# Optimization experiments

Hardware: AMD Instinct MI355X
Metric: run time of the kernel (lower is better)

The kernel has to match this reference:

```python
import jax, jax.numpy as jnp
import numpy as np

B, T, D_MODEL, HEAD_DIM = 16, 4096, 512, 64


def setup_inputs() -> dict:
    key = jax.random.key(0)
    kx, kq, kk, kv = jax.random.split(key, 4)
    x = jax.random.normal(kx, (B, T, D_MODEL), dtype=jnp.float32)
    # torch nn.Linear weights, stored pre-transposed as [in, out] for x @ W
    s = 1.0 / np.sqrt(D_MODEL)
    Wq = jax.random.uniform(kq, (D_MODEL, HEAD_DIM), jnp.float32, -s, s)
    Wk = jax.random.uniform(kk, (D_MODEL, HEAD_DIM), jnp.float32, -s, s)
    Wv = jax.random.uniform(kv, (D_MODEL, HEAD_DIM), jnp.float32, -s, s)
    return {"x": x, "Wq": Wq, "Wk": Wk, "Wv": Wv}


def reference(x, Wq, Wk, Wv):
    # Single-head causal self-attention (dropout in eval mode = identity)
    q = x @ Wq  # [B, T, h]
    k = x @ Wk
    v = x @ Wv
    scale = 1.0 / np.sqrt(HEAD_DIM).astype(np.float32)
    scores = jnp.einsum("bth,bsh->bts", q, k) * scale  # [B, T, T]
    t = scores.shape[1]
    causal = jnp.tril(jnp.ones((t, t), dtype=bool))
    scores = jnp.where(causal, scores, -jnp.inf)
    weights = jax.nn.softmax(scores, axis=-1)
    return jnp.einsum("bts,bsh->bth", weights, v)  # [B, T, h]
```

## Files before the change

### kernel.cpp

```cpp
#include <hip/hip_runtime.h>
#include <hip/hip_bf16.h>
#include <math.h>


#define NB 16
#define NT 4096
#define DMODEL 512
#define HD 64
#define CEXP 0.18033688011112042f

typedef unsigned short u16;
typedef unsigned int u32;
typedef __attribute__((ext_vector_type(2))) unsigned int u32x2;
typedef __attribute__((ext_vector_type(8))) short bf16x8;
typedef __attribute__((ext_vector_type(4))) float f32x4;
typedef __attribute__((ext_vector_type(16))) float f32x16;

__device__ __forceinline__ u16 f2bf(float x) {
  union { float f; unsigned u; } v; v.f = x;
  unsigned r = v.u + 0x7fffu + ((v.u >> 16) & 1u);
  return (u16)(r >> 16);
}

__device__ __forceinline__ u32 cvtpk(float lo, float hi) {
  u32 r;
  asm("v_cvt_pk_bf16_f32 %0, %1, %2" : "=v"(r) : "v"(lo), "v"(hi));
  return r;
}

__device__ __forceinline__ u32x2 lane_swap(u32 a, u32 b) {
  asm("v_permlane32_swap_b32 %0, %1" : "+v"(a), "+v"(b));
  u32x2 r; r[0] = a; r[1] = b; return r;
}

__device__ __forceinline__ void gload16(const void* g, void* l) {
  __builtin_amdgcn_global_load_lds(
      (const __attribute__((address_space(1))) void*)g,
      (__attribute__((address_space(3))) void*)l, 16, 0, 0);
}

#define MFMA32(a, b, c) __builtin_amdgcn_mfma_f32_16x16x32_bf16(a, b, c, 0, 0, 0)
#define WMFMA(a, b, c)  __builtin_amdgcn_mfma_f32_32x32x16_bf16(a, b, c, 0, 0, 0)
#define LD8(p) (*(const bf16x8*)(p))

__global__ void prep_wt(const float* __restrict__ Wq, const float* __restrict__ Wk,
                        const float* __restrict__ Wv, u16* __restrict__ Wt) {
  int k0 = blockIdx.x * 16;
  int t = threadIdx.x;
#pragma unroll
  for (int i = 0; i < 12; ++i) {
    int idx = t + i * 256;
    int n = idx % 192;
    int kk = idx / 192;
    const float* W = (n < 64) ? Wq : (n < 128) ? Wk : Wv;
    float w = W[(size_t)(k0 + kk) * 64 + (n & 63)];
    Wt[(size_t)n * 512 + k0 + kk] = f2bf(w);
  }
}

__global__ __launch_bounds__(512) void proj_qkv(const float* __restrict__ x,
                                                const u16* __restrict__ Wt,
                                                u16* __restrict__ qo,
                                                u16* __restrict__ ko,
                                                u16* __restrict__ vo) {
  __shared__ u16 As[128][48];
  int t = threadIdx.x;
  int m0 = blockIdx.x * 128;
  int lane = t & 63, wid = t >> 6;
  int wr = wid >> 2, wc = wid & 3;
  int g = lane >> 4, li = lane & 15;
  f32x4 acc[4][3];
#pragma unroll
  for (int i = 0; i < 4; ++i)
#pragma unroll
    for (int j = 0; j < 3; ++j) acc[i][j] = (f32x4){0.f, 0.f, 0.f, 0.f};

  int row = t >> 2, quad = t & 3;
  for (int k0 = 0; k0 < 512; k0 += 32) {
    __syncthreads();
    const float* src = x + (size_t)(m0 + row) * DMODEL + k0 + quad * 8;
    float4 f0 = *(const float4*)src;
    float4 f1 = *(const float4*)(src + 4);
    union { u16 s[8]; bf16x8 v; } tmp;
    tmp.s[0] = f2bf(f0.x); tmp.s[1] = f2bf(f0.y);
    tmp.s[2] = f2bf(f0.z); tmp.s[3] = f2bf(f0.w);
    tmp.s[4] = f2bf(f1.x); tmp.s[5] = f2bf(f1.y);
    tmp.s[6] = f2bf(f1.z); tmp.s[7] = f2bf(f1.w);
    *(bf16x8*)&As[row][quad * 8] = tmp.v;
    __syncthreads();

    bf16x8 a[4], bb[3];
#pragma unroll
    for (int mf = 0; mf < 4; ++mf)
      a[mf] = *(const bf16x8*)&As[wr * 64 + mf * 16 + li][g * 8];
#pragma unroll
    for (int nf = 0; nf < 3; ++nf)
      bb[nf] = *(const bf16x8*)(Wt + (size_t)(wc * 48 + nf * 16 + li) * 512 + k0 + g * 8);
#pragma unroll
    for (int mf = 0; mf < 4; ++mf)
#pragma unroll
      for (int nf = 0; nf < 3; ++nf)
        acc[mf][nf] = MFMA32(a[mf], bb[nf], acc[mf][nf]);
  }

#pragma unroll
  for (int nf = 0; nf < 3; ++nf) {
    int n = wc * 48 + nf * 16 + li;
    if (n < 64) {
      int col = n;
#pragma unroll
      for (int mf = 0; mf < 4; ++mf)
#pragma unroll
        for (int r = 0; r < 4; ++r) {
          int m = m0 + wr * 64 + mf * 16 + 4 * g + r;
          qo[(size_t)m * HD + col] = f2bf(acc[mf][nf][r] * CEXP);
        }
    } else if (n < 128) {
      int col = n & 63;
      int dt = col >> 4, hh = (col >> 3) & 1, jj = col & 7;
      size_t fo = (size_t)(dt * 2 + hh) * 256 + jj;
#pragma unroll
      for (int mf = 0; mf < 4; ++mf)
#pragma unroll
        for (int r = 0; r < 4; ++r) {
          int m = m0 + wr * 64 + mf * 16 + 4 * g + r;
          ko[(size_t)(m >> 5) * 2048 + fo + (m & 31) * 8] = f2bf(acc[mf][nf][r]);
        }
    } else {
      int d = n - 128;
      int dh = d >> 5, l31d = d & 31;
#pragma unroll
      for (int mf = 0; mf < 4; ++mf) {
        int mbase = m0 + wr * 64 + mf * 16 + 4 * g;
        int kk2 = mbase & 31;
        int kt2 = kk2 >> 4, hh = (kk2 >> 3) & 1;
        size_t off = (size_t)(mbase >> 5) * 2048 +
                     (size_t)((dh * 2 + kt2) * 2 + hh) * 256 + l31d * 8 + (mbase & 7);
        ushort4 pk;
        pk.x = f2bf(acc[mf][nf][0]);
        pk.y = f2bf(acc[mf][nf][1]);
        pk.z = f2bf(acc[mf][nf][2]);
        pk.w = f2bf(acc[mf][nf][3]);
        *(ushort4*)(vo + off) = pk;
      }
    }
  }
}

__global__ __launch_bounds__(256, 4) void attn_fwd10(const u16* __restrict__ qg,
                                                     const u16* __restrict__ kg,
                                                     const u16* __restrict__ vg,
                                                     float* __restrict__ out) {
  __shared__ __align__(16) char smem[33792];
  u16* KV = (u16*)smem;
  float* MrgF = (float*)smem;

  int tid = threadIdx.x;
  int lane = tid & 63, w = tid >> 6;
  int l31 = lane & 31, h = lane >> 5;
  int qi = w >> 1, ki = w & 1;

  int f = blockIdx.x;
  int xcd = f & 7, i = f >> 3;
  int m = i >> 5, cu = i & 31;
  int b, bp;
  if (m == 0)      { b = 2 * xcd;     bp = 63 - cu; }
  else if (m == 1) { b = 2 * xcd;     bp = 31 - cu; }
  else if (m == 2) { b = 2 * xcd + 1; bp = cu;      }
  else             { b = 2 * xcd + 1; bp = 32 + cu; }

  const int diag = 2 * bp + qi;
  const int nr = bp + 1;
  const int q0w = bp * 64 + qi * 32;

  const u16* qb = qg + (size_t)b * NT * HD;
  const u16* kbs = kg + (size_t)b * NT * HD;
  const u16* vbs = vg + (size_t)b * NT * HD;
  float* ob = out + (size_t)b * NT * HD;

  bf16x8 qf[4];
#pragma unroll
  for (int dt = 0; dt < 4; ++dt)
    qf[dt] = LD8(qb + (size_t)(q0w + l31) * HD + dt * 16 + 8 * h);

  f32x16 oacc0, oacc1;
#pragma unroll
  for (int r = 0; r < 16; ++r) { oacc0[r] = 0.f; oacc1[r] = 0.f; }
  float lsum = 0.f;

  auto COMPUTE = [&](const u16* kp0, const u16* vp0, bool maskdiag) {
    bf16x8 kf[4], vf[4];
#pragma unroll
    for (int dt = 0; dt < 4; ++dt)
      kf[dt] = LD8(kp0 + dt * 512 + h * 256 + l31 * 8);
#pragma unroll
    for (int dv = 0; dv < 4; ++dv)
      vf[dv] = LD8(vp0 + dv * 512 + h * 256 + l31 * 8);

    f32x16 sv;
#pragma unroll
    for (int r = 0; r < 16; ++r) sv[r] = 0.f;
    sv = WMFMA(kf[0], qf[0], sv);
    sv = WMFMA(kf[1], qf[1], sv);
    sv = WMFMA(kf[2], qf[2], sv);
    sv = WMFMA(kf[3], qf[3], sv);

    if (maskdiag) {
#pragma unroll
      for (int r = 0; r < 16; ++r) {
        int key = (r & 3) + 8 * (r >> 2) + 4 * h;
        if (key > l31) sv[r] = -1e30f;
      }
    }

    float p[16];
#pragma unroll
    for (int r = 0; r < 16; ++r) p[r] = __builtin_amdgcn_exp2f(sv[r]);
    lsum += (((p[0] + p[1]) + (p[2] + p[3])) + ((p[4] + p[5]) + (p[6] + p[7]))) +
            (((p[8] + p[9]) + (p[10] + p[11])) + ((p[12] + p[13]) + (p[14] + p[15])));
    u32 A0 = cvtpk(p[0], p[1]),   A1 = cvtpk(p[2], p[3]);
    u32 B0 = cvtpk(p[4], p[5]),   B1 = cvtpk(p[6], p[7]);
    u32 C0 = cvtpk(p[8], p[9]),   C1 = cvtpk(p[10], p[11]);
    u32 E0 = cvtpk(p[12], p[13]), E1 = cvtpk(p[14], p[15]);
    u32x2 s0 = lane_swap(A0, B0), s1 = lane_swap(A1, B1);
    u32x2 s2 = lane_swap(C0, E0), s3 = lane_swap(C1, E1);
    union { u32 d[4]; bf16x8 v; } f0u, f1u;
    f0u.d[0] = s0[0]; f0u.d[1] = s1[0]; f0u.d[2] = s0[1]; f0u.d[3] = s1[1];
    f1u.d[0] = s2[0]; f1u.d[1] = s3[0]; f1u.d[2] = s2[1]; f1u.d[3] = s3[1];

    oacc0 = WMFMA(vf[0], f0u.v, oacc0);
    oacc1 = WMFMA(vf[2], f0u.v, oacc1);
    oacc0 = WMFMA(vf[1], f1u.v, oacc0);
    oacc1 = WMFMA(vf[3], f1u.v, oacc1);
  };

  gload16(kbs + tid * 8,        KV + tid * 8);
  gload16(vbs + tid * 8,        KV + 2048 + tid * 8);
  gload16(kbs + 2048 + tid * 8, KV + 4096 + tid * 8);
  gload16(vbs + 2048 + tid * 8, KV + 6144 + tid * 8);

  int cur = 0;
  for (int jr = 0; jr < nr; ++jr) {
    if (jr + 1 < nr) {
      const u16* gk = kbs + (size_t)(2 * jr + 2) * 2048 + tid * 8;
      const u16* gv = vbs + (size_t)(2 * jr + 2) * 2048 + tid * 8;
      u16* lb = KV + (cur ^ 1) * 8192;
      gload16(gk,        lb + tid * 8);
      gload16(gv,        lb + 2048 + tid * 8);
      gload16(gk + 2048, lb + 4096 + tid * 8);
      gload16(gv + 2048, lb + 6144 + tid * 8);
      asm volatile("s_waitcnt vmcnt(4)" ::: "memory");
    } else {
      asm volatile("s_waitcnt vmcnt(0)" ::: "memory");
    }
    __builtin_amdgcn_sched_barrier(0);
    asm volatile("s_barrier" ::: "memory");

    const u16* kv0 = KV + cur * 8192;
    int jmine = 2 * jr + ki;
    if (jmine <= diag)
      COMPUTE(kv0 + ki * 4096, kv0 + ki * 4096 + 2048, jmine == diag);

    asm volatile("s_barrier" ::: "memory");
    cur ^= 1;
  }

  lsum += __shfl_xor(lsum, 32);
  {
    float* mg = MrgF + ((size_t)w * 64 + lane) * 33;
#pragma unroll
    for (int r = 0; r < 16; ++r) { mg[r] = oacc0[r]; mg[16 + r] = oacc1[r]; }
    mg[32] = lsum;
  }
  __syncthreads();
#pragma unroll
  for (int s = 0; s < 4; ++s) {
    int ql = (lane >> 2) + 16 * (s & 1);
    int dq = ki * 8 + (lane & 3) + 4 * (s >> 1);
    const float* m0p = MrgF + ((size_t)(qi * 2) * 64) * 33;
    const float* m1p = MrgF + ((size_t)(qi * 2 + 1) * 64) * 33;
    float ls = m0p[(size_t)ql * 33 + 32] + m1p[(size_t)ql * 33 + 32];
    float inv = 1.0f / ls;
    f32x4 o4;
#pragma unroll
    for (int dd = 0; dd < 4; ++dd) {
      int d = dq * 4 + dd;
      int dh = d >> 5, rem = d & 31;
      int srch = (rem >> 2) & 1;
      int reg = dh * 16 + (rem & 3) + ((rem >> 3) << 2);
      size_t ro = (size_t)(ql + 32 * srch) * 33 + reg;
      o4[dd] = (m0p[ro] + m1p[ro]) * inv;
    }
    *(f32x4*)(ob + (size_t)(q0w + ql) * HD + dq * 4) = o4;
  }
}

extern "C" void kernel_launch(void* const* d_in, const int* in_sizes, int n_in,
                              void* d_out, int out_size, void* d_ws, size_t ws_size,
                              hipStream_t stream) {
  const float* x  = (const float*)d_in[0];
  const float* Wq = (const float*)d_in[1];
  const float* Wk = (const float*)d_in[2];
  const float* Wv = (const float*)d_in[3];
  float* out = (float*)d_out;

  u16* Wt  = (u16*)d_ws;
  u16* qws = (u16*)((char*)d_ws + 192 * 512 * 2);
  u16* kws = qws + (size_t)NB * NT * HD;
  u16* vws = kws + (size_t)NB * NT * HD;

  prep_wt<<<32, 256, 0, stream>>>(Wq, Wk, Wv, Wt);
  proj_qkv<<<(NB * NT) / 128, 512, 0, stream>>>(x, Wt, qws, kws, vws);
  attn_fwd10<<<1024, 256, 0, stream>>>(qws, kws, vws, out);
}
```

Baseline: 96.75 us.

## Double KV stage depth, prefetch x in projection, and simplify attention block scheduling

The attention kernel now stages four 32-key tiles per iteration into a 64KB double buffer instead of two, which halves the number of barrier rounds. Each wave issues its own tile loads, and compute is wrapped in s_setprio. Launch bounds drop to 2 blocks per SM, and the block-to-(batch, row) mapping becomes a simple heavy-first ordering. The projection kernel software-prefetches x two k-steps ahead and uses the library bf16 conversion instead of the hand-written rounding. The larger LDS footprint lowers occupancy and may hurt latency hiding and load balance.

```diff
diff --git a/kernel.cpp b/kernel.cpp
--- a/kernel.cpp
+++ b/kernel.cpp
@@ -16,10 +16,9 @@
 typedef __attribute__((ext_vector_type(4))) float f32x4;
 typedef __attribute__((ext_vector_type(16))) float f32x16;
 
-__device__ __forceinline__ u16 f2bf(float x) {
-  union { float f; unsigned u; } v; v.f = x;
-  unsigned r = v.u + 0x7fffu + ((v.u >> 16) & 1u);
-  return (u16)(r >> 16);
+__device__ __forceinline__ u16 bfu(float x) {
+  __hip_bfloat16 h = __float2bfloat16(x);
+  return *(u16*)&h;
 }
 
 __device__ __forceinline__ u32 cvtpk(float lo, float hi) {
@@ -54,7 +53,7 @@
     int kk = idx / 192;
     const float* W = (n < 64) ? Wq : (n < 128) ? Wk : Wv;
     float w = W[(size_t)(k0 + kk) * 64 + (n & 63)];
-    Wt[(size_t)n * 512 + k0 + kk] = f2bf(w);
+    Wt[(size_t)n * 512 + k0 + kk] = bfu(w);
   }
 }
 
@@ -76,19 +75,29 @@
     for (int j = 0; j < 3; ++j) acc[i][j] = (f32x4){0.f, 0.f, 0.f, 0.f};
 
   int row = t >> 2, quad = t & 3;
-  for (int k0 = 0; k0 < 512; k0 += 32) {
+  const float* srcb = x + (size_t)(m0 + row) * DMODEL + quad * 8;
+
+  float4 pa0[2], pa1[2];
+  pa0[0] = *(const float4*)(srcb);       pa1[0] = *(const float4*)(srcb + 4);
+  pa0[1] = *(const float4*)(srcb + 32);  pa1[1] = *(const float4*)(srcb + 36);
+
+#pragma unroll
+  for (int s = 0; s < 16; ++s) {
+    float4 c0 = pa0[s & 1], c1 = pa1[s & 1];
+    if (s + 2 < 16) {
+      pa0[s & 1] = *(const float4*)(srcb + (s + 2) * 32);
+      pa1[s & 1] = *(const float4*)(srcb + (s + 2) * 32 + 4);
+    }
     __syncthreads();
-    const float* src = x + (size_t)(m0 + row) * DMODEL + k0 + quad * 8;
-    float4 f0 = *(const float4*)src;
-    float4 f1 = *(const float4*)(src + 4);
-    union { u16 s[8]; bf16x8 v; } tmp;
-    tmp.s[0] = f2bf(f0.x); tmp.s[1] = f2bf(f0.y);
-    tmp.s[2] = f2bf(f0.z); tmp.s[3] = f2bf(f0.w);
-    tmp.s[4] = f2bf(f1.x); tmp.s[5] = f2bf(f1.y);
-    tmp.s[6] = f2bf(f1.z); tmp.s[7] = f2bf(f1.w);
+    union { u16 u[8]; bf16x8 v; } tmp;
+    tmp.u[0] = bfu(c0.x); tmp.u[1] = bfu(c0.y);
+    tmp.u[2] = bfu(c0.z); tmp.u[3] = bfu(c0.w);
+    tmp.u[4] = bfu(c1.x); tmp.u[5] = bfu(c1.y);
+    tmp.u[6] = bfu(c1.z); tmp.u[7] = bfu(c1.w);
     *(bf16x8*)&As[row][quad * 8] = tmp.v;
     __syncthreads();
 
+    int k0 = s * 32;
     bf16x8 a[4], bb[3];
 #pragma unroll
     for (int mf = 0; mf < 4; ++mf)
@@ -113,7 +122,7 @@
 #pragma unroll
         for (int r = 0; r < 4; ++r) {
           int m = m0 + wr * 64 + mf * 16 + 4 * g + r;
-          qo[(size_t)m * HD + col] = f2bf(acc[mf][nf][r] * CEXP);
+          qo[(size_t)m * HD + col] = bfu(acc[mf][nf][r] * CEXP);
         }
     } else if (n < 128) {
       int col = n & 63;
@@ -124,7 +133,7 @@
 #pragma unroll
         for (int r = 0; r < 4; ++r) {
           int m = m0 + wr * 64 + mf * 16 + 4 * g + r;
-          ko[(size_t)(m >> 5) * 2048 + fo + (m & 31) * 8] = f2bf(acc[mf][nf][r]);
+          ko[(size_t)(m >> 5) * 2048 + fo + (m & 31) * 8] = bfu(acc[mf][nf][r]);
         }
     } else {
       int d = n - 128;
@@ -137,21 +146,21 @@
         size_t off = (size_t)(mbase >> 5) * 2048 +
                      (size_t)((dh * 2 + kt2) * 2 + hh) * 256 + l31d * 8 + (mbase & 7);
         ushort4 pk;
-        pk.x = f2bf(acc[mf][nf][0]);
-        pk.y = f2bf(acc[mf][nf][1]);
-        pk.z = f2bf(acc[mf][nf][2]);
-        pk.w = f2bf(acc[mf][nf][3]);
+        pk.x = bfu(acc[mf][nf][0]);
+        pk.y = bfu(acc[mf][nf][1]);
+        pk.z = bfu(acc[mf][nf][2]);
+        pk.w = bfu(acc[mf][nf][3]);
         *(ushort4*)(vo + off) = pk;
       }
     }
   }
 }
 
-__global__ __launch_bounds__(256, 4) void attn_fwd10(const u16* __restrict__ qg,
+__global__ __launch_bounds__(256, 2) void attn_fwd11(const u16* __restrict__ qg,
                                                      const u16* __restrict__ kg,
                                                      const u16* __restrict__ vg,
                                                      float* __restrict__ out) {
-  __shared__ __align__(16) char smem[33792];
+  __shared__ __align__(16) char smem[65536];
   u16* KV = (u16*)smem;
   float* MrgF = (float*)smem;
 
@@ -162,15 +171,12 @@
 
   int f = blockIdx.x;
   int xcd = f & 7, i = f >> 3;
-  int m = i >> 5, cu = i & 31;
-  int b, bp;
-  if (m == 0)      { b = 2 * xcd;     bp = 63 - cu; }
-  else if (m == 1) { b = 2 * xcd;     bp = 31 - cu; }
-  else if (m == 2) { b = 2 * xcd + 1; bp = cu;      }
-  else             { b = 2 * xcd + 1; bp = 32 + cu; }
-
-  const int diag = 2 * bp + qi;
-  const int nr = bp + 1;
+  int b = 2 * xcd + (i & 1);
+  int bp = 63 - (i >> 1);
+
+  const int limb = 2 * bp + 1;
+  const int diagw = 2 * bp + qi;
+  const int nr = (bp + 2) >> 1;
   const int q0w = bp * 64 + qi * 32;
 
   const u16* qb = qg + (size_t)b * NT * HD;
@@ -187,6 +193,17 @@
 #pragma unroll
   for (int r = 0; r < 16; ++r) { oacc0[r] = 0.f; oacc1[r] = 0.f; }
   float lsum = 0.f;
+
+  auto STAGE = [&](u16* lb, int tg) {
+    const u16* gk = kbs + (size_t)tg * 2048 + lane * 8;
+    const u16* gv = vbs + (size_t)tg * 2048 + lane * 8;
+    u16* dk = lb + w * 4096 + lane * 8;
+#pragma unroll
+    for (int ii = 0; ii < 4; ++ii) {
+      gload16(gk + ii * 512, dk + ii * 512);
+      gload16(gv + ii * 512, dk + 2048 + ii * 512);
+    }
+  };
 
   auto COMPUTE = [&](const u16* kp0, const u16* vp0, bool maskdiag) {
     bf16x8 kf[4], vf[4];
@@ -234,32 +251,27 @@
     oacc1 = WMFMA(vf[3], f1u.v, oacc1);
   };
 
-  gload16(kbs + tid * 8,        KV + tid * 8);
-  gload16(vbs + tid * 8,        KV + 2048 + tid * 8);
-  gload16(kbs + 2048 + tid * 8, KV + 4096 + tid * 8);
-  gload16(vbs + 2048 + tid * 8, KV + 6144 + tid * 8);
+  STAGE(KV, min(w, limb));
 
   int cur = 0;
   for (int jr = 0; jr < nr; ++jr) {
     if (jr + 1 < nr) {
-      const u16* gk = kbs + (size_t)(2 * jr + 2) * 2048 + tid * 8;
-      const u16* gv = vbs + (size_t)(2 * jr + 2) * 2048 + tid * 8;
-      u16* lb = KV + (cur ^ 1) * 8192;
-      gload16(gk,        lb + tid * 8);
-      gload16(gv,        lb + 2048 + tid * 8);
-      gload16(gk + 2048, lb + 4096 + tid * 8);
-      gload16(gv + 2048, lb + 6144 + tid * 8);
-      asm volatile("s_waitcnt vmcnt(4)" ::: "memory");
+      STAGE(KV + (cur ^ 1) * 16384, min(4 * (jr + 1) + w, limb));
+      asm volatile("s_waitcnt vmcnt(8)" ::: "memory");
     } else {
       asm volatile("s_waitcnt vmcnt(0)" ::: "memory");
     }
     __builtin_amdgcn_sched_barrier(0);
     asm volatile("s_barrier" ::: "memory");
 
-    const u16* kv0 = KV + cur * 8192;
-    int jmine = 2 * jr + ki;
-    if (jmine <= diag)
-      COMPUTE(kv0 + ki * 4096, kv0 + ki * 4096 + 2048, jmine == diag);
+    const u16* kv0 = KV + cur * 16384;
+    int j1 = 4 * jr + ki, j2 = 4 * jr + 2 + ki;
+    __builtin_amdgcn_s_setprio(1);
+    if (j1 <= diagw)
+      COMPUTE(kv0 + ki * 4096, kv0 + ki * 4096 + 2048, j1 == diagw);
+    if (j2 <= diagw)
+      COMPUTE(kv0 + (2 + ki) * 4096, kv0 + (2 + ki) * 4096 + 2048, j2 == diagw);
+    __builtin_amdgcn_s_setprio(0);
 
     asm volatile("s_barrier" ::: "memory");
     cur ^= 1;
@@ -311,5 +323,5 @@
 
   prep_wt<<<32, 256, 0, stream>>>(Wq, Wk, Wv, Wt);
   proj_qkv<<<(NB * NT) / 128, 512, 0, stream>>>(x, Wt, qws, kws, vws);
-  attn_fwd10<<<1024, 256, 0, stream>>>(qws, kws, vws, out);
-}
+  attn_fwd11<<<1024, 256, 0, stream>>>(qws, kws, vws, out);
+}
```

Result: faster. 91.39 us (-5.5%).
